# Kernel optimization log

Measured on AMD Instinct MI355X. Metric: run time of the kernel, lower is better.

## Reference

```python
import jax, jax.numpy as jnp
import numpy as np

B, N, C, R = 4, 4096, 64, 16
EPS = 1e-12


def setup_inputs() -> dict:
    key = jax.random.key(0)
    k_x, k_w, k_u = jax.random.split(key, 3)
    x = jax.random.normal(k_x, (B, N, C), dtype=jnp.float32)
    W = jax.random.uniform(k_w, (B, N, N), dtype=jnp.float32)
    # lazily-initialized learnable low-rank factor U ~ 0.01 * randn(N, r)
    U = 0.01 * jax.random.normal(k_u, (N, R), dtype=jnp.float32)
    w_scale = jnp.asarray(1.0, dtype=jnp.float32)
    return {"x": x, "W": W, "U": U, "w_scale": w_scale}


def reference(x, W, U, w_scale):
    # symmetrize adjacency: W <- (W + W^T)/2
    Ws = 0.5 * (W + jnp.swapaxes(W, -1, -2))            # [B,N,N]
    # low-rank symmetric gate A = sigmoid(U U^T), shared over batch
    A = jax.nn.sigmoid(U @ U.T)                          # [N,N]
    K = Ws * A[None, :, :]                               # [B,N,N]
    # degree normalization K <- D^{-1/2} K D^{-1/2}
    # (diag_embed + two bmms in the original == row/col broadcast scaling)
    deg = jnp.maximum(K.sum(axis=-1), EPS)               # [B,N]
    d = jax.lax.rsqrt(deg)                               # [B,N]
    K = K * d[:, :, None] * d[:, None, :]                # [B,N,N]
    # coupling: w_scale * K @ x
    return w_scale * jnp.einsum('bnm,bmc->bnc', K, x)    # [B,N,C]
```

## Files before the change

kernel.cpp:

```cpp
#include <hip/hip_runtime.h>
#include <hip/hip_bf16.h>

#define B_ 4
#define N_ 4096
#define C_ 64
#define R_ 16
#define EPS_ 1e-12f

typedef __attribute__((ext_vector_type(8))) short bf16x8;
typedef __attribute__((ext_vector_type(4))) float f32x4;

static __device__ __forceinline__ unsigned short f2bf(float f) {
    unsigned int u = __float_as_uint(f);
    unsigned int r = (u + 0x7fffu + ((u >> 16) & 1u)) >> 16;
    return (unsigned short)r;
}
static __device__ __forceinline__ float bf2f(unsigned short us) {
    return __uint_as_float(((unsigned int)us) << 16);
}

static __device__ __forceinline__ size_t k0f_off(int b, int rt, int k32, int fq, int fr) {
    return ((((size_t)(b * 256 + rt)) * 128 + k32) * 4 + fq) * 128 + fr * 8;
}

__global__ __launch_bounds__(256) void k_pass1(
    const float* __restrict__ W, const float* __restrict__ U,
    unsigned short* __restrict__ K0, float* __restrict__ deg)
{
    const int tj = blockIdx.x, ti = blockIdx.y;
    if (ti > tj) return;
    const int I = ti * 64, J = tj * 64;
    const bool diag = (ti == tj);
    const int t = threadIdx.x;
    const int ii = t >> 2, g = t & 3, jjg = g * 16;

    __shared__ float UJ[64][17];
    __shared__ float Wc[64][65];
    __shared__ __align__(16) unsigned short K0s[64][72];

    {
        const float4 v = *(const float4*)(U + (size_t)(J + (t >> 2)) * R_ + (t & 3) * 4);
        UJ[t >> 2][(t & 3) * 4 + 0] = v.x;
        UJ[t >> 2][(t & 3) * 4 + 1] = v.y;
        UJ[t >> 2][(t & 3) * 4 + 2] = v.z;
        UJ[t >> 2][(t & 3) * 4 + 3] = v.w;
    }

    float4 wcv[4], wrv[4], wcvN[4], wrvN[4];
    #pragma unroll
    for (int k = 0; k < 4; k++) {
        const int idx = t + 256 * k, row = idx >> 4, c4 = idx & 15;
        wcv[k] = *(const float4*)(W + ((size_t)(0 * N_ + J + row)) * N_ + I + c4 * 4);
    }
    #pragma unroll
    for (int h = 0; h < 4; h++)
        wrv[h] = *(const float4*)(W + ((size_t)(0 * N_ + I + ii)) * N_ + J + jjg + 4 * h);

    float ui[16];
    {
        const float* up = U + (size_t)(I + ii) * R_;
        #pragma unroll
        for (int h = 0; h < 4; h++) {
            float4 v = *(const float4*)(up + 4 * h);
            ui[4*h] = v.x; ui[4*h+1] = v.y; ui[4*h+2] = v.z; ui[4*h+3] = v.w;
        }
    }
    __syncthreads();

    float a[16];
    #pragma unroll
    for (int q = 0; q < 16; q++) {
        float s = 0.f;
        #pragma unroll
        for (int k = 0; k < 16; k++) s += ui[k] * UJ[jjg + q][k];
        a[q] = 1.0f / (1.0f + __expf(-s));
    }

    #pragma unroll
    for (int k = 0; k < 4; k++) {
        const int idx = t + 256 * k, row = idx >> 4, c4 = idx & 15;
        Wc[row][c4*4+0] = wcv[k].x; Wc[row][c4*4+1] = wcv[k].y;
        Wc[row][c4*4+2] = wcv[k].z; Wc[row][c4*4+3] = wcv[k].w;
    }
    __syncthreads();

    for (int b = 0; b < B_; b++) {
        if (b < B_ - 1) {
            #pragma unroll
            for (int k = 0; k < 4; k++) {
                const int idx = t + 256 * k, row = idx >> 4, c4 = idx & 15;
                wcvN[k] = *(const float4*)(W + ((size_t)((b+1) * N_ + J + row)) * N_ + I + c4 * 4);
            }
            #pragma unroll
            for (int h = 0; h < 4; h++)
                wrvN[h] = *(const float4*)(W + ((size_t)((b+1) * N_ + I + ii)) * N_ + J + jjg + 4 * h);
        }

        const float* wrf = (const float*)wrv;
        float sumI = 0.f;
        unsigned int pk[8];
        #pragma unroll
        for (int q = 0; q < 16; q++) {
            float k0 = 0.5f * (wrf[q] + Wc[jjg + q][ii]) * a[q];
            sumI += k0;
            unsigned short us = f2bf(k0);
            if (q & 1) pk[q >> 1] |= ((unsigned int)us) << 16;
            else       pk[q >> 1] = us;
        }
        *(int4*)(&K0s[ii][jjg])     = make_int4(pk[0], pk[1], pk[2], pk[3]);
        *(int4*)(&K0s[ii][jjg + 8]) = make_int4(pk[4], pk[5], pk[6], pk[7]);
        {
            const int rt  = (I + ii) >> 4, fr = ii & 15;
            const int k32 = (J >> 5) + (g >> 1), fqa = (g & 1) * 2;
            unsigned short* dst = K0 + k0f_off(b, rt, k32, fqa, fr);
            *(int4*)(dst)       = make_int4(pk[0], pk[1], pk[2], pk[3]);
            *(int4*)(dst + 128) = make_int4(pk[4], pk[5], pk[6], pk[7]);
        }
        {
            float s = sumI + __shfl_xor(sumI, 1, 64);
            s += __shfl_xor(s, 2, 64);
            if (g == 0) atomicAdd(deg + b * N_ + I + ii, s);
        }
        __syncthreads();

        if (!diag) {
            const int c2 = t & 31, r8 = t >> 5;
            unsigned int v[8];
            float cs0 = 0.f, cs1 = 0.f;
            #pragma unroll
            for (int k = 0; k < 8; k++) {
                v[k] = *(const unsigned int*)(&K0s[r8 * 8 + k][c2 * 2]);
                cs0 += bf2f((unsigned short)(v[k] & 0xffffu));
                cs1 += bf2f((unsigned short)(v[k] >> 16));
            }
            unsigned int plo[4], phi[4];
            #pragma unroll
            for (int m = 0; m < 4; m++) {
                plo[m] = (v[2*m] & 0xffffu) | (v[2*m+1] << 16);
                phi[m] = (v[2*m] >> 16) | (v[2*m+1] & 0xffff0000u);
            }
            const int rtp  = (J >> 4) + (c2 >> 3), fr0 = (2 * c2) & 15;
            const int k32p = (I >> 5) + (r8 >> 2), fqp = r8 & 3;
            unsigned short* dst0 = K0 + k0f_off(b, rtp, k32p, fqp, fr0);
            *(int4*)(dst0)     = make_int4(plo[0], plo[1], plo[2], plo[3]);
            *(int4*)(dst0 + 8) = make_int4(phi[0], phi[1], phi[2], phi[3]);
            cs0 += __shfl_xor(cs0, 32, 64);
            cs1 += __shfl_xor(cs1, 32, 64);
            if ((t & 32) == 0) {
                atomicAdd(deg + b * N_ + J + 2 * c2,     cs0);
                atomicAdd(deg + b * N_ + J + 2 * c2 + 1, cs1);
            }
        }
        if (b < B_ - 1) {
            #pragma unroll
            for (int k = 0; k < 4; k++) {
                const int idx = t + 256 * k, row = idx >> 4, c4 = idx & 15;
                Wc[row][c4*4+0] = wcvN[k].x; Wc[row][c4*4+1] = wcvN[k].y;
                Wc[row][c4*4+2] = wcvN[k].z; Wc[row][c4*4+3] = wcvN[k].w;
            }
            #pragma unroll
            for (int h = 0; h < 4; h++) wrv[h] = wrvN[h];
            __syncthreads();
        }
    }
}

__global__ __launch_bounds__(256) void k_xdT(
    const float* __restrict__ x, const float* __restrict__ deg,
    unsigned short* __restrict__ xdT)
{
    const int jt = blockIdx.x, b = blockIdx.y;
    const int J = jt * 64, t = threadIdx.x;
    __shared__ float xt[64][69];
    #pragma unroll
    for (int k = 0; k < 4; k++) {
        int idx = t + 256 * k;
        int row = idx >> 4, f4 = idx & 15;
        float d = rsqrtf(fmaxf(deg[b * N_ + J + row], EPS_));
        float4 v = *(const float4*)(x + ((size_t)(b * N_ + J + row)) * C_ + f4 * 4);
        xt[row][f4*4+0] = v.x * d; xt[row][f4*4+1] = v.y * d;
        xt[row][f4*4+2] = v.z * d; xt[row][f4*4+3] = v.w * d;
    }
    __syncthreads();
    #pragma unroll
    for (int p = 0; p < 2; p++) {
        const int linear = p * 256 + t;
        const int k32h = linear >> 8, rem = linear & 255;
        const int cg = rem >> 6, l = rem & 63, fq = l >> 4, fr = l & 15;
        const int c = cg * 16 + fr;
        const int jb = k32h * 32 + fq * 8;
        unsigned int pk[4];
        #pragma unroll
        for (int m = 0; m < 4; m++) {
            pk[m] = (unsigned int)f2bf(xt[jb + 2*m][c]) |
                    ((unsigned int)f2bf(xt[jb + 2*m + 1][c]) << 16);
        }
        unsigned short* dst = xdT +
            (((size_t)(b * 128 + (J >> 5) + k32h)) * 4 + cg) * 512 + l * 8;
        *(int4*)dst = make_int4(pk[0], pk[1], pk[2], pk[3]);
    }
}

__global__ __launch_bounds__(256) void k_gemm(
    const unsigned short* __restrict__ K0, const unsigned short* __restrict__ xdT,
    const float* __restrict__ deg, const float* __restrict__ wsc_p,
    float* __restrict__ out)
{
    const int rb = blockIdx.x, b = blockIdx.y;
    const int t = threadIdx.x, l = t & 63, w = t >> 6;
    const int rt = rb * 4 + w;

    const unsigned short* Ap = K0  + (size_t)(b * 256 + rt) * 65536 + l * 8;
    const unsigned short* Bp = xdT + (size_t)b * 262144 + l * 8;

    f32x4 acc0 = {0.f,0.f,0.f,0.f}, acc1 = {0.f,0.f,0.f,0.f};
    f32x4 acc2 = {0.f,0.f,0.f,0.f}, acc3 = {0.f,0.f,0.f,0.f};

    #pragma unroll 4
    for (int k32 = 0; k32 < 128; k32++) {
        bf16x8 av = *(const bf16x8*)(Ap + (size_t)k32 * 512);
        bf16x8 b0 = *(const bf16x8*)(Bp + (size_t)k32 * 2048);
        bf16x8 b1 = *(const bf16x8*)(Bp + (size_t)k32 * 2048 + 512);
        bf16x8 b2 = *(const bf16x8*)(Bp + (size_t)k32 * 2048 + 1024);
        bf16x8 b3 = *(const bf16x8*)(Bp + (size_t)k32 * 2048 + 1536);
        acc0 = __builtin_amdgcn_mfma_f32_16x16x32_bf16(av, b0, acc0, 0, 0, 0);
        acc1 = __builtin_amdgcn_mfma_f32_16x16x32_bf16(av, b1, acc1, 0, 0, 0);
        acc2 = __builtin_amdgcn_mfma_f32_16x16x32_bf16(av, b2, acc2, 0, 0, 0);
        acc3 = __builtin_amdgcn_mfma_f32_16x16x32_bf16(av, b3, acc3, 0, 0, 0);
    }

    const int fr = l & 15, fq = l >> 4;
    const float wsc = wsc_p[0];
    #pragma unroll
    for (int r = 0; r < 4; r++) {
        const int row = rt * 16 + fq * 4 + r;
        const float sc = wsc * rsqrtf(fmaxf(deg[b * N_ + row], EPS_));
        float* op = out + ((size_t)(b * N_ + row)) * C_;
        op[fr]      = sc * acc0[r];
        op[16 + fr] = sc * acc1[r];
        op[32 + fr] = sc * acc2[r];
        op[48 + fr] = sc * acc3[r];
    }
}

extern "C" void kernel_launch(void* const* d_in, const int* in_sizes, int n_in,
                              void* d_out, int out_size, void* d_ws, size_t ws_size,
                              hipStream_t stream)
{
    const float* x   = (const float*)d_in[0];
    const float* W   = (const float*)d_in[1];
    const float* U   = (const float*)d_in[2];
    const float* wsc = (const float*)d_in[3];
    float* out = (float*)d_out;

    unsigned short* K0  = (unsigned short*)d_ws;
    float*          deg = (float*)((char*)d_ws + (size_t)B_ * N_ * N_ * 2);
    unsigned short* xdT = (unsigned short*)((char*)deg + (size_t)B_ * N_ * 4);

    hipMemsetAsync(deg, 0, (size_t)B_ * N_ * sizeof(float), stream);
    hipLaunchKernelGGL(k_pass1, dim3(64, 64), dim3(256), 0, stream, W, U, K0, deg);
    hipLaunchKernelGGL(k_xdT,  dim3(64, 4),  dim3(256), 0, stream, x, deg, xdT);
    hipLaunchKernelGGL(k_gemm, dim3(64, 4),  dim3(256), 0, stream, K0, xdT, deg, wsc, out);
}
```

Measured before the change: 463.5 us.

## Split GEMM K dimension across blocks with atomic accumulation

The GEMM kernel now uses single-wave blocks, each covering one 16-row tile and one quarter of the K range. Partial results are combined with atomicAdd into an output that is zeroed beforehand. The goal is to raise the number of concurrently running waves, since the GEMM previously launched only 256 blocks of 4 waves each. In exchange it adds a memset of the output, float atomics, and a summation order that is no longer deterministic.

```diff
diff --git a/kernel.cpp b/kernel.cpp
--- a/kernel.cpp
+++ b/kernel.cpp
@@ -201,28 +201,30 @@
     }
 }
 
-__global__ __launch_bounds__(256) void k_gemm(
+__global__ __launch_bounds__(64, 4) void k_gemm(
     const unsigned short* __restrict__ K0, const unsigned short* __restrict__ xdT,
     const float* __restrict__ deg, const float* __restrict__ wsc_p,
     float* __restrict__ out)
 {
-    const int rb = blockIdx.x, b = blockIdx.y;
-    const int t = threadIdx.x, l = t & 63, w = t >> 6;
-    const int rt = rb * 4 + w;
-
-    const unsigned short* Ap = K0  + (size_t)(b * 256 + rt) * 65536 + l * 8;
-    const unsigned short* Bp = xdT + (size_t)b * 262144 + l * 8;
+    const int blk = blockIdx.x, b = blockIdx.y;
+    const int rt = blk >> 2, kq = blk & 3;
+    const int l = threadIdx.x;
+
+    const unsigned short* Ap = K0  + (size_t)(b * 256 + rt) * 65536
+                                   + (size_t)(kq * 32) * 512 + l * 8;
+    const unsigned short* Bp = xdT + (size_t)b * 262144
+                                   + (size_t)(kq * 32) * 2048 + l * 8;
 
     f32x4 acc0 = {0.f,0.f,0.f,0.f}, acc1 = {0.f,0.f,0.f,0.f};
     f32x4 acc2 = {0.f,0.f,0.f,0.f}, acc3 = {0.f,0.f,0.f,0.f};
 
     #pragma unroll 4
-    for (int k32 = 0; k32 < 128; k32++) {
-        bf16x8 av = *(const bf16x8*)(Ap + (size_t)k32 * 512);
-        bf16x8 b0 = *(const bf16x8*)(Bp + (size_t)k32 * 2048);
-        bf16x8 b1 = *(const bf16x8*)(Bp + (size_t)k32 * 2048 + 512);
-        bf16x8 b2 = *(const bf16x8*)(Bp + (size_t)k32 * 2048 + 1024);
-        bf16x8 b3 = *(const bf16x8*)(Bp + (size_t)k32 * 2048 + 1536);
+    for (int k = 0; k < 32; k++) {
+        bf16x8 av = *(const bf16x8*)(Ap + (size_t)k * 512);
+        bf16x8 b0 = *(const bf16x8*)(Bp + (size_t)k * 2048);
+        bf16x8 b1 = *(const bf16x8*)(Bp + (size_t)k * 2048 + 512);
+        bf16x8 b2 = *(const bf16x8*)(Bp + (size_t)k * 2048 + 1024);
+        bf16x8 b3 = *(const bf16x8*)(Bp + (size_t)k * 2048 + 1536);
         acc0 = __builtin_amdgcn_mfma_f32_16x16x32_bf16(av, b0, acc0, 0, 0, 0);
         acc1 = __builtin_amdgcn_mfma_f32_16x16x32_bf16(av, b1, acc1, 0, 0, 0);
         acc2 = __builtin_amdgcn_mfma_f32_16x16x32_bf16(av, b2, acc2, 0, 0, 0);
@@ -236,10 +238,10 @@
         const int row = rt * 16 + fq * 4 + r;
         const float sc = wsc * rsqrtf(fmaxf(deg[b * N_ + row], EPS_));
         float* op = out + ((size_t)(b * N_ + row)) * C_;
-        op[fr]      = sc * acc0[r];
-        op[16 + fr] = sc * acc1[r];
-        op[32 + fr] = sc * acc2[r];
-        op[48 + fr] = sc * acc3[r];
+        atomicAdd(op + fr,      sc * acc0[r]);
+        atomicAdd(op + 16 + fr, sc * acc1[r]);
+        atomicAdd(op + 32 + fr, sc * acc2[r]);
+        atomicAdd(op + 48 + fr, sc * acc3[r]);
     }
 }
 
@@ -258,7 +260,8 @@
     unsigned short* xdT = (unsigned short*)((char*)deg + (size_t)B_ * N_ * 4);
 
     hipMemsetAsync(deg, 0, (size_t)B_ * N_ * sizeof(float), stream);
+    hipMemsetAsync(out, 0, (size_t)B_ * N_ * C_ * sizeof(float), stream);
     hipLaunchKernelGGL(k_pass1, dim3(64, 64), dim3(256), 0, stream, W, U, K0, deg);
-    hipLaunchKernelGGL(k_xdT,  dim3(64, 4),  dim3(256), 0, stream, x, deg, xdT);
-    hipLaunchKernelGGL(k_gemm, dim3(64, 4),  dim3(256), 0, stream, K0, xdT, deg, wsc, out);
-}
+    hipLaunchKernelGGL(k_xdT,  dim3(64, 4),   dim3(256), 0, stream, x, deg, xdT);
+    hipLaunchKernelGGL(k_gemm, dim3(1024, 4), dim3(64),  0, stream, K0, xdT, deg, wsc, out);
+}
```

After: 458.3 us. Within noise of the previous version (-1.1%).
